# Kernel optimization log

Hardware: AMD Instinct MI355X
Metric: run time of the kernel (lower is better)

The kernel has to match this reference:

```python
import jax, jax.numpy as jnp
import numpy as np

MIN_CURV = 1e-06
MIN_NORM = 1e-15

def _norm(x):
    return jnp.clip(jnp.linalg.norm(x, axis=-1, keepdims=True), MIN_NORM, None)

def lorentz_expmap0(v, c):
    sqrt_c = jnp.sqrt(c)
    vn = _norm(v)
    x0 = jnp.cosh(sqrt_c * vn) / sqrt_c
    xs = jnp.sinh(sqrt_c * vn) * v / (sqrt_c * vn)
    return jnp.concatenate([x0, xs], axis=-1)

def lorentz_logmap0(x, c):
    sqrt_c = jnp.sqrt(c)
    x0 = x[..., 0:1]
    xs = x[..., 1:]
    xs_norm = _norm(xs)
    theta = jnp.arccosh(jnp.clip(sqrt_c * x0, 1.0 + 1e-07, None))
    return theta / (sqrt_c * xs_norm) * xs

def lorentz_project(x, c):
    spatial = x[..., 1:]
    sq = jnp.sum(spatial * spatial, axis=-1, keepdims=True)
    x0 = jnp.clip(jnp.sqrt(sq + 1.0 / c), MIN_NORM, None)
    return jnp.concatenate([x0, spatial], axis=-1)

def givens_rotation(x, angles):
    x0 = x[..., 0:1]
    xs = x[..., 1:]
    cos_a = jnp.cos(angles)
    sin_a = jnp.sin(angles)
    xe = xs[..., 0::2]
    xo = xs[..., 1::2]
    ne = cos_a * xe - sin_a * xo
    no = sin_a * xe + cos_a * xo
    xr = jnp.stack([ne, no], axis=-1).reshape(xs.shape)
    return jnp.concatenate([x0, xr], axis=-1)

def setup_inputs() -> dict:
    key = jax.random.key(0)
    ks = jax.random.split(key, 16)
    N_NODE, E, B = 50000, 500000, 64
    IN_DIM, OUT_DIM, ATTN_DIM, N_REL = 128, 128, 128, 200
    N_EMB = 2 * N_REL + 1  # 401
    hidden = jax.random.normal(ks[0], (N_NODE, IN_DIM), dtype=jnp.float32)
    q_sub = jax.random.randint(ks[1], (B,), 0, N_NODE)
    q_rel = jax.random.randint(ks[2], (B,), 0, N_EMB)
    r_idx = jax.random.randint(ks[3], (E,), 0, B)
    rel = jax.random.randint(ks[4], (E,), 0, N_EMB)
    sub = jax.random.randint(ks[5], (E,), 0, N_NODE)
    obj = jax.random.randint(ks[6], (E,), 0, N_NODE)
    zeros = jnp.zeros((E,), dtype=jnp.int32)
    edges = jnp.stack([r_idx, zeros, rel, zeros, sub, obj], axis=1)
    rela_embed = jax.random.normal(ks[7], (N_EMB, IN_DIM), dtype=jnp.float32)
    rel_angles = jax.random.uniform(ks[8], (N_EMB, IN_DIM // 2), minval=-0.1, maxval=0.1, dtype=jnp.float32)
    curvature = jnp.array(1.0, dtype=jnp.float32)
    Ws_w = jax.random.normal(ks[9], (ATTN_DIM, IN_DIM), dtype=jnp.float32) * 0.05
    Wr_w = jax.random.normal(ks[10], (ATTN_DIM, IN_DIM), dtype=jnp.float32) * 0.05
    Wqr_w = jax.random.normal(ks[11], (ATTN_DIM, IN_DIM), dtype=jnp.float32) * 0.05
    Wqr_b = jax.random.normal(ks[12], (ATTN_DIM,), dtype=jnp.float32) * 0.05
    Wattn_w = jax.random.normal(ks[13], (1, ATTN_DIM), dtype=jnp.float32) * 0.05
    Wh_w = jax.random.normal(ks[14], (OUT_DIM, IN_DIM), dtype=jnp.float32) * 0.05
    return {"hidden": hidden, "rela_embed": rela_embed, "rel_angles": rel_angles,
            "curvature": curvature, "Ws_w": Ws_w, "Wr_w": Wr_w, "Wqr_w": Wqr_w,
            "Wqr_b": Wqr_b, "Wattn_w": Wattn_w, "Wh_w": Wh_w,
            "q_sub": q_sub, "q_rel": q_rel, "edges": edges,
            "n_node": N_NODE, "old_nodes_new_idx": jnp.arange(N_NODE)}

def reference(hidden, rela_embed, rel_angles, curvature, Ws_w, Wr_w, Wqr_w, Wqr_b,
              Wattn_w, Wh_w, q_sub, q_rel, edges, n_node, old_nodes_new_idx):
    sub = edges[:, 4]
    rel = edges[:, 2]
    obj = edges[:, 5]
    r_idx = edges[:, 0]
    hs = hidden[sub]                      # [E, in_dim]
    hr = rela_embed[rel]                  # [E, in_dim]
    h_qr = rela_embed[q_rel][r_idx]       # [E, in_dim]
    pre = jax.nn.relu(hs @ Ws_w.T + hr @ Wr_w.T + h_qr @ Wqr_w.T + Wqr_b)
    alpha = jax.nn.sigmoid(pre @ Wattn_w.T)  # [E, 1]
    c = jnp.clip(curvature, MIN_CURV, None)
    mess_tangent = hs + hr
    mess_L = lorentz_expmap0(mess_tangent, c)          # [E, in_dim+1]
    mess_L = givens_rotation(mess_L, rel_angles[rel])
    mess2 = lorentz_logmap0(mess_L, c)                 # [E, in_dim]
    message = mess2 * alpha
    message_agg = jax.ops.segment_sum(message, obj, num_segments=n_node)
    a = message_agg @ Wh_w.T                           # [n_node, out_dim]
    a_L = lorentz_expmap0(a, c)
    # act is identity; project back to hyperboloid and log-map
    a_L = lorentz_project(jnp.concatenate([a_L[..., 0:1], a_L[..., 1:]], axis=-1), c)
    hidden_new = lorentz_logmap0(a_L, c)
    return hidden_new
```

## Files before the change

### kernel.cpp

```cpp
#include <hip/hip_runtime.h>
#include <math.h>

#define D 128
#define CAP 36

typedef _Float16 f16x8 __attribute__((ext_vector_type(8)));
typedef _Float16 f16x4 __attribute__((ext_vector_type(4)));
typedef _Float16 f16x2 __attribute__((ext_vector_type(2)));
typedef float    f32x4 __attribute__((ext_vector_type(4)));

union H8 { f16x8 v; f16x4 q[2]; f16x2 p[4]; _Float16 f[8]; };
union H4 { f16x4 v; f16x2 p[2]; _Float16 f[4]; };

__device__ __forceinline__ float fdot2f(f16x2 a, f16x2 b, float c){
  return __builtin_amdgcn_fdot2(a, b, c, false);
}
__device__ __forceinline__ f16x2 relu2(f16x2 x){
  f16x2 r;
  r[0] = x[0] > (_Float16)0 ? x[0] : (_Float16)0;
  r[1] = x[1] > (_Float16)0 ? x[1] : (_Float16)0;
  return r;
}
__device__ __forceinline__ float rsum32(float v){
  v += __shfl_xor(v, 16);
  v += __shfl_xor(v, 8);
  v += __shfl_xor(v, 4);
  v += __shfl_xor(v, 2);
  v += __shfl_xor(v, 1);
  return v;
}


__device__ __forceinline__ void hgemm_core16(const _Float16* __restrict__ A,
                                             const _Float16* __restrict__ W,
                                             int arow, f32x4 acc[8], int quad, int lo){
  #pragma unroll
  for (int kt=0;kt<4;kt++){
    f16x8 a = *(const f16x8*)(A + (size_t)arow*D + kt*32 + quad*8);
    #pragma unroll
    for (int nt=0;nt<8;nt++){
      f16x8 b = *(const f16x8*)(W + (size_t)(nt*16 + lo)*D + kt*32 + quad*8);
      acc[nt] = __builtin_amdgcn_mfma_f32_16x16x32_f16(a, b, acc[nt], 0, 0, 0);
    }
  }
}

__device__ __forceinline__ void store_wpart(_Float16* __restrict__ O, f32x4 acc[8],
                                            int m0, int quad, int lo, int M){
  int r0 = m0 + quad*4;
  #pragma unroll
  for (int i=0;i<4;i++){
    int r = r0 + i;
    if (r < M){
      H4 s1, s2;
      #pragma unroll
      for (int nt=0;nt<4;nt++){
        s1.f[nt] = (_Float16)acc[nt][i];
        s2.f[nt] = (_Float16)acc[nt+4][i];
      }
      *(f16x4*)(O + (size_t)r*256 + lo*16 + 4)  = s1.v;
      *(f16x4*)(O + (size_t)r*256 + lo*16 + 12) = s2.v;
    }
  }
}

__global__ __launch_bounds__(256) void k_prep(
    const float* __restrict__ rela, const float* __restrict__ rel_angles,
    const float* __restrict__ Ws, const float* __restrict__ Wr,
    const float* __restrict__ Wh, const float* __restrict__ Wqr,
    const float* __restrict__ Wqr_b, const int* __restrict__ q_rel,
    _Float16* __restrict__ rela16, _Float16* __restrict__ relhq,
    _Float16* __restrict__ relcs, _Float16* __restrict__ Ws16,
    _Float16* __restrict__ Wr16, _Float16* __restrict__ Wh16,
    _Float16* __restrict__ hqw16, int* __restrict__ cnt,
    int NEMB, int NN, int PA){
  __shared__ float emb[D];
  int b = blockIdx.x;
  int t = threadIdx.x;
  if (b < PA){
    int idx = b*256 + t;
    int T1 = NEMB*32;
    if (idx < T1){
      int r = idx >> 5, l = idx & 31;
      float4 hv = *(const float4*)(rela + (size_t)r*D + l*4);
      f16x4 h = { (_Float16)hv.x, (_Float16)hv.y, (_Float16)hv.z, (_Float16)hv.w };
      *(f16x4*)(rela16 + (size_t)r*D + l*4) = h;
      *(f16x4*)(relhq  + (size_t)r*256 + l*8) = h;
      float2 an = *(const float2*)(rel_angles + (size_t)r*(D/2) + l*2);
      float c0 = cosf(an.x), s0 = sinf(an.x);
      float c1 = cosf(an.y), s1 = sinf(an.y);
      H8 cs;
      cs.f[0]=(_Float16)c0; cs.f[1]=(_Float16)(-s0); cs.f[2]=(_Float16)s0; cs.f[3]=(_Float16)c0;
      cs.f[4]=(_Float16)c1; cs.f[5]=(_Float16)(-s1); cs.f[6]=(_Float16)s1; cs.f[7]=(_Float16)c1;
      *(f16x8*)(relcs + (size_t)r*256 + l*8) = cs.v;
      return;
    }
    int j = idx - T1;
    if (j < 3*D*D/4){
      const float* src = (j < 4096) ? Ws : (j < 8192) ? Wr : Wh;
      _Float16*    dst = (j < 4096) ? Ws16 : (j < 8192) ? Wr16 : Wh16;
      int o = (j & 4095)*4;
      float4 v = *(const float4*)(src + o);
      f16x4 h = { (_Float16)v.x, (_Float16)v.y, (_Float16)v.z, (_Float16)v.w };
      *(f16x4*)(dst + o) = h;
      return;
    }
    j -= 3*D*D/4;
    if (j < NN) cnt[j] = 0;
  } else {
    int bb = b - PA;
    if (t < D) emb[t] = rela[(size_t)q_rel[bb]*D + t];
    __syncthreads();
    if (t < D){
      float acc = Wqr_b[t];
      #pragma unroll 8
      for (int k=0;k<D;k++) acc += emb[k]*Wqr[t*D + k];
      int p = ((t & 15) << 3) + (t >> 4);
      hqw16[bb*D + p] = (_Float16)acc;
    }
  }
}

__global__ __launch_bounds__(256) void k_mega(
    const int* __restrict__ edges, int* __restrict__ cnt, int* __restrict__ bucket,
    int E, const float* __restrict__ hidden, const _Float16* __restrict__ Ws16,
    _Float16* __restrict__ hw16, int NN,
    const _Float16* __restrict__ rela16, const _Float16* __restrict__ Wr16,
    _Float16* __restrict__ relhq, int NEMB, int SB, int GH){
  int b = blockIdx.x;
  if (b < SB){
    int e0 = (b*256 + threadIdx.x)*4;
    if (e0 >= E) return;
    if (e0 + 3 < E){
      const int4* q = (const int4*)(edges + (size_t)e0*6);
      int4 q0=q[0], q1=q[1], q2=q[2], q3=q[3], q4=q[4], q5=q[5];
      int key0 = q1.x | (q0.z << 17) | (q0.x << 26);
      int key1 = q2.z | (q2.x << 17) | (q1.z << 26);
      int key2 = q4.x | (q3.z << 17) | (q3.x << 26);
      int key3 = q5.z | (q5.x << 17) | (q4.z << 26);
      int p0 = atomicAdd(cnt + q1.y, 1);
      int p1 = atomicAdd(cnt + q2.w, 1);
      int p2 = atomicAdd(cnt + q4.y, 1);
      int p3 = atomicAdd(cnt + q5.w, 1);
      if (p0 < CAP) bucket[q1.y*CAP + p0] = key0;
      if (p1 < CAP) bucket[q2.w*CAP + p1] = key1;
      if (p2 < CAP) bucket[q4.y*CAP + p2] = key2;
      if (p3 < CAP) bucket[q5.w*CAP + p3] = key3;
    } else {
      for (int u=0; u<4; u++){
        int e = e0 + u;
        if (e < E){
          const int* er = edges + (size_t)e*6;
          int key = er[4] | (er[2] << 17) | (er[0] << 26);
          int pos = atomicAdd(cnt + er[5], 1);
          if (pos < CAP) bucket[er[5]*CAP + pos] = key;
        }
      }
    }
  } else if (b < SB + GH){
    int bb = b - SB;
    int wave = threadIdx.x >> 6;
    int lane = threadIdx.x & 63;
    int quad = lane >> 4, lo = lane & 15;
    int m0 = bb*64 + wave*16;
    int arow = min(m0 + lo, NN-1);
    f32x4 acc[8];
    #pragma unroll
    for (int nt=0;nt<8;nt++) acc[nt] = (f32x4){0.f,0.f,0.f,0.f};
    H8 hpack[4];
    #pragma unroll
    for (int kt=0;kt<4;kt++){
      float4 a0 = *(const float4*)(hidden + (size_t)arow*D + kt*32 + quad*8);
      float4 a1 = *(const float4*)(hidden + (size_t)arow*D + kt*32 + quad*8 + 4);
      H8 a;
      a.f[0]=(_Float16)a0.x; a.f[1]=(_Float16)a0.y; a.f[2]=(_Float16)a0.z; a.f[3]=(_Float16)a0.w;
      a.f[4]=(_Float16)a1.x; a.f[5]=(_Float16)a1.y; a.f[6]=(_Float16)a1.z; a.f[7]=(_Float16)a1.w;
      hpack[kt] = a;
      #pragma unroll
      for (int nt=0;nt<8;nt++){
        f16x8 bb2 = *(const f16x8*)(Ws16 + (size_t)(nt*16 + lo)*D + kt*32 + quad*8);
        acc[nt] = __builtin_amdgcn_mfma_f32_16x16x32_f16(a.v, bb2, acc[nt], 0, 0, 0);
      }
    }
    if (m0 + lo < NN){
      #pragma unroll
      for (int kt=0;kt<4;kt++){
        int g = kt*8 + quad*2;
        *(f16x4*)(hw16 + (size_t)arow*256 + g*8)     = hpack[kt].q[0];
        *(f16x4*)(hw16 + (size_t)arow*256 + (g+1)*8) = hpack[kt].q[1];
      }
    }
    store_wpart(hw16, acc, m0, quad, lo, NN);
  } else {
    int bb = b - SB - GH;
    int wave = threadIdx.x >> 6;
    int lane = threadIdx.x & 63;
    int quad = lane >> 4, lo = lane & 15;
    int m0 = bb*64 + wave*16;
    int arow = min(m0 + lo, NEMB-1);
    f32x4 acc[8];
    #pragma unroll
    for (int nt=0;nt<8;nt++) acc[nt] = (f32x4){0.f,0.f,0.f,0.f};
    hgemm_core16(rela16, Wr16, arow, acc, quad, lo);
    store_wpart(relhq, acc, m0, quad, lo, NEMB);
  }
}

__device__ __forceinline__ void edge_op(int key,
    const _Float16* __restrict__ hw16, const _Float16* __restrict__ relcs,
    const _Float16* __restrict__ relhq, const _Float16* __restrict__ hqw16,
    unsigned lh8, unsigned lh4, f16x2 wa01, f16x2 wa23,
    float& ax, float& ay, float& az, float& aw){
  unsigned sub = key & 0x1FFFF, rel = ((unsigned)key >> 17) & 0x1FF, ri = (unsigned)key >> 26;
  H8 hw; hw.v = *(const f16x8*)(hw16  + (sub << 8) + lh8);
  H8 cs; cs.v = *(const f16x8*)(relcs + (rel << 8) + lh8);
  H8 hq; hq.v = *(const f16x8*)(relhq + (rel << 8) + lh8);
  H4 qw; qw.v = *(const f16x4*)(hqw16 + (ri  << 7) + lh4);
  f16x2 t01 = relu2(hw.p[2] + hq.p[2] + qw.p[0]);
  f16x2 t23 = relu2(hw.p[3] + hq.p[3] + qw.p[1]);
  float s = fdot2f(t01, wa01, fdot2f(t23, wa23, 0.f));
  s = rsum32(s);
  float al = __builtin_amdgcn_rcpf(1.f + __expf(-s));
  f16x2 v01 = hw.p[0] + hq.p[0];
  f16x2 v23 = hw.p[1] + hq.p[1];
  ax += al * fdot2f(cs.p[0], v01, 0.f);
  ay += al * fdot2f(cs.p[1], v01, 0.f);
  az += al * fdot2f(cs.p[2], v23, 0.f);
  aw += al * fdot2f(cs.p[3], v23, 0.f);
}

#define ASTR 136

__global__ __launch_bounds__(256) void k_aggfin(
    const _Float16* __restrict__ hw16, const _Float16* __restrict__ relcs,
    const _Float16* __restrict__ relhq, const _Float16* __restrict__ hqw16,
    const float* __restrict__ Wattn, const int* __restrict__ cnt,
    const int* __restrict__ bucket, const _Float16* __restrict__ Wh16,
    float* __restrict__ out, int NN){
  __shared__ _Float16 As[16*ASTR];
  int t = threadIdx.x;
  int half = t >> 5, l = t & 31;
  unsigned lh8 = (unsigned)l*8, lh4 = (unsigned)l*4;
  unsigned p0 = (unsigned)l*4;
  float w0 = Wattn[(((p0+0)&7)<<4) + ((p0+0)>>3)];
  float w1 = Wattn[(((p0+1)&7)<<4) + ((p0+1)>>3)];
  float w2 = Wattn[(((p0+2)&7)<<4) + ((p0+2)>>3)];
  float w3 = Wattn[(((p0+3)&7)<<4) + ((p0+3)>>3)];
  f16x2 wa01 = { (_Float16)w0, (_Float16)w1 };
  f16x2 wa23 = { (_Float16)w2, (_Float16)w3 };

  int nbase = blockIdx.x * 8;
  int n = nbase + half;
  float ax=0.f, ay=0.f, az=0.f, aw=0.f;
  if (n < NN){
    int deg = min(cnt[n], CAP);
    const int* bk = bucket + n*CAP;
    int i = 0;
    for (; i+4 <= deg; i += 4){
      int4 q = *(const int4*)(bk + i);
      edge_op(q.x, hw16, relcs, relhq, hqw16, lh8, lh4, wa01, wa23, ax, ay, az, aw);
      edge_op(q.y, hw16, relcs, relhq, hqw16, lh8, lh4, wa01, wa23, ax, ay, az, aw);
      edge_op(q.z, hw16, relcs, relhq, hqw16, lh8, lh4, wa01, wa23, ax, ay, az, aw);
      edge_op(q.w, hw16, relcs, relhq, hqw16, lh8, lh4, wa01, wa23, ax, ay, az, aw);
    }
    for (; i < deg; i++)
      edge_op(bk[i], hw16, relcs, relhq, hqw16, lh8, lh4, wa01, wa23, ax, ay, az, aw);
  }
  H4 o;
  o.f[0] = (_Float16)ax; o.f[1] = (_Float16)ay;
  o.f[2] = (_Float16)az; o.f[3] = (_Float16)aw;
  *(f16x4*)(As + half*ASTR + lh4) = o.v;
  __syncthreads();

  int wv = t >> 6, lane = t & 63;
  int quad = lane >> 4, lo = lane & 15;
  f32x4 acc[2];
  acc[0] = (f32x4){0.f,0.f,0.f,0.f};
  acc[1] = (f32x4){0.f,0.f,0.f,0.f};
  #pragma unroll
  for (int kt=0;kt<4;kt++){
    f16x8 a = *(const f16x8*)(As + lo*ASTR + kt*32 + quad*8);
    #pragma unroll
    for (int u=0;u<2;u++){
      int nt = wv*2 + u;
      f16x8 b = *(const f16x8*)(Wh16 + (size_t)(nt*16 + lo)*D + kt*32 + quad*8);
      acc[u] = __builtin_amdgcn_mfma_f32_16x16x32_f16(a, b, acc[u], 0, 0, 0);
    }
  }
  #pragma unroll
  for (int u=0;u<2;u++){
    int c = (wv*2 + u)*16 + lo;
    #pragma unroll
    for (int i=0;i<4;i++){
      int rr = quad*4 + i;
      int r = nbase + rr;
      if (rr < 8 && r < NN) out[(size_t)r*D + c] = acc[u][i];
    }
  }
}

extern "C" void kernel_launch(void* const* d_in, const int* in_sizes, int n_in,
                              void* d_out, int out_size, void* d_ws, size_t ws_size,
                              hipStream_t stream){
  const float* hidden     = (const float*)d_in[0];
  const float* rela       = (const float*)d_in[1];
  const float* rel_angles = (const float*)d_in[2];
  const float* Ws         = (const float*)d_in[4];
  const float* Wr         = (const float*)d_in[5];
  const float* Wqr        = (const float*)d_in[6];
  const float* Wqr_b      = (const float*)d_in[7];
  const float* Wattn      = (const float*)d_in[8];
  const float* Wh         = (const float*)d_in[9];
  const int*   q_rel      = (const int*)d_in[11];
  const int*   edges      = (const int*)d_in[12];

  int NN   = in_sizes[0] / D;
  int NEMB = in_sizes[1] / D;
  int B    = in_sizes[11];
  int E    = in_sizes[12] / 6;

  char* p = (char*)d_ws;
  auto alloc = [&](size_t bytes)->char*{
    char* r = p; p += (bytes + 255) & ~(size_t)255; return r;
  };
  _Float16* hw16   = (_Float16*)alloc((size_t)NN*256*2);
  _Float16* rela16 = (_Float16*)alloc((size_t)NEMB*D*2);
  _Float16* relhq  = (_Float16*)alloc((size_t)NEMB*256*2);
  _Float16* relcs  = (_Float16*)alloc((size_t)NEMB*256*2);
  _Float16* hqw16  = (_Float16*)alloc((size_t)B*D*2);
  _Float16* Ws16   = (_Float16*)alloc((size_t)D*D*2);
  _Float16* Wr16   = (_Float16*)alloc((size_t)D*D*2);
  _Float16* Wh16   = (_Float16*)alloc((size_t)D*D*2);
  int*      cnt    = (int*)alloc((size_t)NN*4);
  int*      bucket = (int*)alloc((size_t)NN*CAP*4);

  int smallN = NEMB*32 + 3*D*D/4 + NN;
  int PA = (smallN + 255)/256;
  k_prep<<<PA + B, 256, 0, stream>>>(rela, rel_angles, Ws, Wr, Wh, Wqr, Wqr_b,
                                     q_rel, rela16, relhq, relcs, Ws16, Wr16,
                                     Wh16, hqw16, cnt, NEMB, NN, PA);

  int SB = (E + 1023)/1024;
  int GH = (NN + 63)/64;
  int G1 = (NEMB + 63)/64;
  k_mega<<<SB + GH + G1, 256, 0, stream>>>(edges, cnt, bucket, E, hidden, Ws16,
                                           hw16, NN, rela16, Wr16, relhq, NEMB,
                                           SB, GH);

  k_aggfin<<<(NN+7)/8, 256, 0, stream>>>(hw16, relcs, relhq, hqw16, Wattn,
                                         cnt, bucket, Wh16, (float*)d_out, NN);
}
```

Before: 241.4 us.

## Mask edge tail and give each wave a private slab for the Wh GEMM

The per-node edge loop now always processes groups of four, multiplying each attention weight by a 0/1 mask instead of running a scalar remainder loop, which keeps control flow uniform. The block-wide __syncthreads before the output GEMM is removed. Each wave now writes its two nodes' aggregated messages to its own shared-memory slab and computes all 8 output column tiles itself, with only rows 0-1 of each MFMA meaningful. This removes cross-wave synchronisation but does four times the MFMA work per wave and reads Wh fully in every wave. It may also read bucket entries past deg, which can hold garbage keys that index out of range; they are masked only after the loads.

```diff
diff --git a/kernel.cpp b/kernel.cpp
--- a/kernel.cpp
+++ b/kernel.cpp
@@ -206,7 +206,7 @@
   }
 }
 
-__device__ __forceinline__ void edge_op(int key,
+__device__ __forceinline__ void edge_op(int key, float msk,
     const _Float16* __restrict__ hw16, const _Float16* __restrict__ relcs,
     const _Float16* __restrict__ relhq, const _Float16* __restrict__ hqw16,
     unsigned lh8, unsigned lh4, f16x2 wa01, f16x2 wa23,
@@ -220,7 +220,7 @@
   f16x2 t23 = relu2(hw.p[3] + hq.p[3] + qw.p[1]);
   float s = fdot2f(t01, wa01, fdot2f(t23, wa23, 0.f));
   s = rsum32(s);
-  float al = __builtin_amdgcn_rcpf(1.f + __expf(-s));
+  float al = msk * __builtin_amdgcn_rcpf(1.f + __expf(-s));
   f16x2 v01 = hw.p[0] + hq.p[0];
   f16x2 v23 = hw.p[1] + hq.p[1];
   ax += al * fdot2f(cs.p[0], v01, 0.f);
@@ -237,7 +237,7 @@
     const float* __restrict__ Wattn, const int* __restrict__ cnt,
     const int* __restrict__ bucket, const _Float16* __restrict__ Wh16,
     float* __restrict__ out, int NN){
-  __shared__ _Float16 As[16*ASTR];
+  __shared__ _Float16 As[4*2*ASTR];
   int t = threadIdx.x;
   int half = t >> 5, l = t & 31;
   unsigned lh8 = (unsigned)l*8, lh4 = (unsigned)l*4;
@@ -255,46 +255,45 @@
   if (n < NN){
     int deg = min(cnt[n], CAP);
     const int* bk = bucket + n*CAP;
-    int i = 0;
-    for (; i+4 <= deg; i += 4){
+    for (int i = 0; i < deg; i += 4){
       int4 q = *(const int4*)(bk + i);
-      edge_op(q.x, hw16, relcs, relhq, hqw16, lh8, lh4, wa01, wa23, ax, ay, az, aw);
-      edge_op(q.y, hw16, relcs, relhq, hqw16, lh8, lh4, wa01, wa23, ax, ay, az, aw);
-      edge_op(q.z, hw16, relcs, relhq, hqw16, lh8, lh4, wa01, wa23, ax, ay, az, aw);
-      edge_op(q.w, hw16, relcs, relhq, hqw16, lh8, lh4, wa01, wa23, ax, ay, az, aw);
-    }
-    for (; i < deg; i++)
-      edge_op(bk[i], hw16, relcs, relhq, hqw16, lh8, lh4, wa01, wa23, ax, ay, az, aw);
-  }
+      int rem = deg - i;
+      edge_op(q.x, 1.f,                  hw16, relcs, relhq, hqw16, lh8, lh4, wa01, wa23, ax, ay, az, aw);
+      edge_op(q.y, rem > 1 ? 1.f : 0.f,  hw16, relcs, relhq, hqw16, lh8, lh4, wa01, wa23, ax, ay, az, aw);
+      edge_op(q.z, rem > 2 ? 1.f : 0.f,  hw16, relcs, relhq, hqw16, lh8, lh4, wa01, wa23, ax, ay, az, aw);
+      edge_op(q.w, rem > 3 ? 1.f : 0.f,  hw16, relcs, relhq, hqw16, lh8, lh4, wa01, wa23, ax, ay, az, aw);
+    }
+  }
+  int wv = half >> 1;
+  _Float16* slab = As + wv*2*ASTR;
   H4 o;
   o.f[0] = (_Float16)ax; o.f[1] = (_Float16)ay;
   o.f[2] = (_Float16)az; o.f[3] = (_Float16)aw;
-  *(f16x4*)(As + half*ASTR + lh4) = o.v;
-  __syncthreads();
-
-  int wv = t >> 6, lane = t & 63;
+  *(f16x4*)(slab + (half & 1)*ASTR + lh4) = o.v;
+
+  int lane = t & 63;
   int quad = lane >> 4, lo = lane & 15;
-  f32x4 acc[2];
-  acc[0] = (f32x4){0.f,0.f,0.f,0.f};
-  acc[1] = (f32x4){0.f,0.f,0.f,0.f};
+  const _Float16* arow_p = slab + (lo < 1 ? 0 : (lo < 2 ? ASTR : ASTR));
+  arow_p = slab + min(lo, 1)*ASTR;
+  f32x4 acc2[8];
+  #pragma unroll
+  for (int nt=0;nt<8;nt++) acc2[nt] = (f32x4){0.f,0.f,0.f,0.f};
   #pragma unroll
   for (int kt=0;kt<4;kt++){
-    f16x8 a = *(const f16x8*)(As + lo*ASTR + kt*32 + quad*8);
-    #pragma unroll
-    for (int u=0;u<2;u++){
-      int nt = wv*2 + u;
+    f16x8 a = *(const f16x8*)(arow_p + kt*32 + quad*8);
+    #pragma unroll
+    for (int nt=0;nt<8;nt++){
       f16x8 b = *(const f16x8*)(Wh16 + (size_t)(nt*16 + lo)*D + kt*32 + quad*8);
-      acc[u] = __builtin_amdgcn_mfma_f32_16x16x32_f16(a, b, acc[u], 0, 0, 0);
-    }
-  }
-  #pragma unroll
-  for (int u=0;u<2;u++){
-    int c = (wv*2 + u)*16 + lo;
-    #pragma unroll
-    for (int i=0;i<4;i++){
-      int rr = quad*4 + i;
-      int r = nbase + rr;
-      if (rr < 8 && r < NN) out[(size_t)r*D + c] = acc[u][i];
+      acc2[nt] = __builtin_amdgcn_mfma_f32_16x16x32_f16(a, b, acc2[nt], 0, 0, 0);
+    }
+  }
+  if (quad == 0){
+    int n0 = nbase + wv*2;
+    #pragma unroll
+    for (int nt=0;nt<8;nt++){
+      int c = nt*16 + lo;
+      if (n0     < NN) out[(size_t)n0*D + c]     = acc2[nt][0];
+      if (n0 + 1 < NN) out[(size_t)(n0+1)*D + c] = acc2[nt][1];
     }
   }
 }
```

New measurement: 305.8 us. 1.27x slower.
